# Kernel tuning notes

Measured on AMD Instinct MI355X. Metric: run time of the kernel, lower is better.

Reference implementation:

```python
import jax, jax.numpy as jnp
import numpy as np

# batch, nodes, input_dim, hid_dim, max_diffusion_step
B, N, C, D, K = 256, 512, 2, 64, 2


def setup_inputs() -> dict:
    key = jax.random.key(0)
    ks = jax.random.split(key, 7)
    F = C + D  # 66
    return {
        "inputs": jax.random.normal(ks[0], (B, N * C), jnp.float32),
        "state": jax.random.normal(ks[1], (B, N * D), jnp.float32),
        "adj": jax.random.uniform(ks[2], (N, N), jnp.float32),
        "W_gate": jax.random.normal(ks[3], (F * (K + 1), 2 * D), jnp.float32) * 0.05,
        "b_gate": jax.random.normal(ks[4], (2 * D,), jnp.float32) * 0.05,
        "W_cand": jax.random.normal(ks[5], (F * (K + 1), D), jnp.float32) * 0.05,
        "b_cand": jax.random.normal(ks[6], (D,), jnp.float32) * 0.05,
    }


def _diffusion_conv(x, adj, W, b):
    # x: (B, N, F) node features; Chebyshev-style diffusion basis then dense projection.
    b_, n_, f_ = x.shape
    k1 = W.shape[0] // f_  # num_matrices = max_diffusion_step + 1
    x0 = x.transpose(1, 2, 0).reshape(n_, f_ * b_)  # (N, F*B)
    xs = [x0]
    if k1 > 1:
        x1 = adj @ x0
        xs.append(x1)
        prev2, prev = x0, x1
        for _ in range(2, k1):
            cur = 2.0 * (adj @ prev) - prev2  # x2 = 2*adj@x1 - x0 recurrence
            xs.append(cur)
            prev2, prev = prev, cur
    stk = jnp.stack(xs, 0).reshape(k1, n_, f_, b_)  # (K+1, N, F, B)
    stk = stk.transpose(3, 1, 2, 0).reshape(b_ * n_, f_ * k1)  # (B*N, F*(K+1))
    out = stk @ W + b  # (B*N, O)
    return out.reshape(b_, n_ * W.shape[1])


def _random_walk_T(adj):
    a = adj + jnp.eye(adj.shape[0], dtype=adj.dtype)
    d = a.sum(axis=1)
    d_inv = jnp.where(d > 0, 1.0 / d, 0.0)
    return (d_inv[:, None] * a).T  # transposed random-walk matrix


def reference(inputs, state, adj, W_gate, b_gate, W_cand, b_cand):
    adj_rw = _random_walk_T(adj)
    inp3 = inputs.reshape(B, N, C)
    st3 = state.reshape(B, N, D)
    xg = jnp.concatenate([inp3, st3], axis=2)  # (B, N, C+D)
    value = jax.nn.sigmoid(_diffusion_conv(xg, adj_rw, W_gate, b_gate))
    value = value.reshape(B, N, 2 * D)
    r, u = value[..., :D], value[..., D:]
    u = u.reshape(B, N * D)
    xc = jnp.concatenate([inp3, r * st3], axis=2)
    c = jnp.tanh(_diffusion_conv(xc, adj_rw, W_cand, b_cand))  # (B, N*D)
    new_state = u * state + (1.0 - u) * c
    return new_state
```

## Files before the change

### kernel.cpp

```cpp
#include <hip/hip_runtime.h>
#include <math.h>

typedef unsigned short u16;
typedef float f32x4 __attribute__((ext_vector_type(4)));
typedef short s16x4 __attribute__((ext_vector_type(4)));
typedef short s16x8 __attribute__((ext_vector_type(8)));

#define AS3 __attribute__((address_space(3)))
#define AS1 __attribute__((address_space(1)))

__device__ __forceinline__ u16 f2bf(float f) {
  unsigned x = __builtin_bit_cast(unsigned, f);
  x += 0x7fffu + ((x >> 16) & 1u);
  return (u16)(x >> 16);
}
__device__ __forceinline__ float bf2f(u16 u) {
  unsigned x = ((unsigned)u) << 16;
  return __builtin_bit_cast(float, x);
}
__device__ __forceinline__ void gload16(const void* g, void* l) {
  __builtin_amdgcn_global_load_lds((const AS1 void*)g, (AS3 void*)l, 16, 0, 0);
}

__global__ void k_dinv(const float* __restrict__ adj, float* __restrict__ dinv) {
  int j = blockIdx.x;
  float s = 0.0f;
  for (int i = threadIdx.x; i < 512; i += 64) s += adj[(size_t)j * 512 + i];
  #pragma unroll
  for (int off = 32; off > 0; off >>= 1) s += __shfl_down(s, off);
  if (threadIdx.x == 0) dinv[j] = 1.0f / (1.0f + s);
}

__global__ void k_buildA(const float* __restrict__ adj, const float* __restrict__ dinv,
                         u16* __restrict__ Ab) {
  int i = blockIdx.x;
  for (int j = threadIdx.x; j < 512; j += 256) {
    float v = adj[(size_t)j * 512 + i] + ((i == j) ? 1.0f : 0.0f);
    Ab[(size_t)i * 512 + j] = f2bf(v * dinv[j]);
  }
}

__global__ __launch_bounds__(256) void k_prepST(const float* __restrict__ s,
                                                u16* __restrict__ Xn,
                                                u16* __restrict__ Xt) {
  __shared__ float Tl[64][65];
  const int b = blockIdx.y, n0 = blockIdx.x * 64;
  const int tid = threadIdx.x;
  const int r = tid >> 4, c4 = (tid & 15) * 4;
  #pragma unroll
  for (int i = 0; i < 4; ++i) {
    f32x4 v = *(const f32x4*)&s[((size_t)b * 512 + n0 + i * 16 + r) * 64 + c4];
    s16x4 o;
    #pragma unroll
    for (int j = 0; j < 4; ++j) { Tl[c4 + j][i * 16 + r] = v[j]; o[j] = (short)f2bf(v[j]); }
    *(s16x4*)&Xn[((size_t)b * 512 + n0 + i * 16 + r) * 64 + c4] = o;
  }
  __syncthreads();
  #pragma unroll
  for (int i = 0; i < 4; ++i) {
    int d = i * 16 + r;
    s16x4 o;
    #pragma unroll
    for (int j = 0; j < 4; ++j) o[j] = (short)f2bf(Tl[d][c4 + j]);
    *(s16x4*)&Xt[((size_t)b * 64 + d) * 512 + n0 + c4] = o;
  }
}

__global__ void k_prepI(const float* __restrict__ inp, u16* __restrict__ Xi0t) {
  const int b = blockIdx.x, t = threadIdx.x;
  const int m2 = t * 2;
  f32x4 v = *(const f32x4*)&inp[(size_t)b * 1024 + m2 * 2];
  unsigned p0 = (unsigned)f2bf(v.x) | ((unsigned)f2bf(v.z) << 16);
  unsigned p1 = (unsigned)f2bf(v.y) | ((unsigned)f2bf(v.w) << 16);
  *(unsigned*)&Xi0t[((size_t)b * 2 + 0) * 512 + m2] = p0;
  *(unsigned*)&Xi0t[((size_t)b * 2 + 1) * 512 + m2] = p1;
}

template<int NC>
__global__ void k_wtp(const float* __restrict__ W, u16* __restrict__ WTp) {
  int col = blockIdx.x, tid = threadIdx.x;
  if (tid >= 224) return;
  int kt = tid >> 5, g = (tid >> 3) & 3, j = tid & 7;
  int kappa = 32 * kt + 4 * g + ((j < 4) ? j : j + 12);
  float v = 0.0f;
  if (kappa < 192) {
    int f = kappa & 63, k1 = kappa >> 6;
    v = W[(size_t)((f + 2) * 3 + k1) * NC + col];
  } else if (kappa < 198) {
    int t = kappa - 192, k1 = t >> 1, c = t & 1;
    v = W[(size_t)(c * 3 + k1) * NC + col];
  }
  WTp[(size_t)col * 224 + tid] = f2bf(v);
}

template<int EPI, int WTB, int WNB>
__global__ __launch_bounds__(256, 3) void k_diffB(const u16* __restrict__ Xt,
                                                  const u16* __restrict__ Ab,
                                                  const u16* __restrict__ X0t,
                                                  u16* __restrict__ Yt,
                                                  u16* __restrict__ Yn) {
  __shared__ __align__(16) u16 SB[16384];
  const int tid = threadIdx.x;
  const int w = tid >> 6, l = tid & 63, g = l >> 4, l16 = l & 15;
  const int Rg = w >> 1, ng = w & 1;
  const int nt0 = blockIdx.x * 128;
  const size_t R0 = (size_t)blockIdx.y * 128;
  const bool isInput = (R0 >= 16384);
  f32x4 acc[4][4] = {};

#define STAGE(BUF, M0)                                                            \
  {                                                                               \
    _Pragma("unroll")                                                             \
    for (int i_ = 0; i_ < 2; ++i_) {                                              \
      int s_ = i_ * 256 + tid, r_ = s_ >> 2, p_ = s_ & 3;                         \
      gload16(&Xt[(R0 + r_) * 512 + (M0) + 8 * (p_ ^ (r_ & 3))],                  \
              &SB[(BUF) * 4096 + s_ * 8]);                                        \
      gload16(&Ab[(size_t)(nt0 + r_) * 512 + (M0) + 8 * (p_ ^ (r_ & 3))],         \
              &SB[8192 + (BUF) * 4096 + s_ * 8]);                                 \
    }                                                                             \
  }

  STAGE(0, 0);
  #pragma unroll
  for (int it = 0; it < 16; ++it) {
    const int cur = it & 1;
    if (it < 15) {
      if (cur == 0) STAGE(1, (it + 1) * 32)
      else          STAGE(0, (it + 1) * 32)
      asm volatile("s_waitcnt vmcnt(4)" ::: "memory");
    } else {
      asm volatile("s_waitcnt vmcnt(0)" ::: "memory");
    }
    __builtin_amdgcn_s_barrier();
    __builtin_amdgcn_sched_barrier(0);

    const u16* XL = &SB[cur * 4096];
    const u16* AL = &SB[8192 + cur * 4096];
    s16x8 af[4], bf[4];
    #pragma unroll
    for (int mt = 0; mt < 4; ++mt) {
      int r = Rg * 64 + mt * 16 + l16;
      const char* rowp = (const char*)XL + r * 64 + 8 * (g & 1);
      int c0 = (g >> 1), c1 = c0 + 2;
      s16x4 lo = *(const s16x4*)(rowp + 16 * (c0 ^ (r & 3)));
      s16x4 hi = *(const s16x4*)(rowp + 16 * (c1 ^ (r & 3)));
      af[mt] = __builtin_shufflevector(lo, hi, 0, 1, 2, 3, 4, 5, 6, 7);
    }
    #pragma unroll
    for (int nt = 0; nt < 4; ++nt) {
      int r = ng * 64 + nt * 16 + l16;
      const char* rowp = (const char*)AL + r * 64 + 8 * (g & 1);
      int c0 = (g >> 1), c1 = c0 + 2;
      s16x4 lo = *(const s16x4*)(rowp + 16 * (c0 ^ (r & 3)));
      s16x4 hi = *(const s16x4*)(rowp + 16 * (c1 ^ (r & 3)));
      bf[nt] = __builtin_shufflevector(lo, hi, 0, 1, 2, 3, 4, 5, 6, 7);
    }
    #pragma unroll
    for (int mt = 0; mt < 4; ++mt)
      #pragma unroll
      for (int nt = 0; nt < 4; ++nt)
        acc[mt][nt] = __builtin_amdgcn_mfma_f32_16x16x32_bf16(af[mt], bf[nt],
                                                              acc[mt][nt], 0, 0, 0);
    __builtin_amdgcn_s_barrier();
    __builtin_amdgcn_sched_barrier(0);
  }
#undef STAGE

  if (EPI) {
    #pragma unroll
    for (int i = 0; i < 8; ++i) {
      int s = i * 256 + tid, r = s >> 4, c = s & 15;
      gload16(&X0t[(R0 + r) * 512 + nt0 + c * 8], &SB[s * 8]);
    }
    asm volatile("s_waitcnt vmcnt(0)" ::: "memory");
    __builtin_amdgcn_s_barrier();
    #pragma unroll
    for (int mt = 0; mt < 4; ++mt)
      #pragma unroll
      for (int nt = 0; nt < 4; ++nt) {
        int nl = ng * 64 + nt * 16 + l16;
        #pragma unroll
        for (int rr = 0; rr < 4; ++rr) {
          int Rl = Rg * 64 + mt * 16 + 4 * g + rr;
          acc[mt][nt][rr] = 2.0f * acc[mt][nt][rr] - bf2f(SB[Rl * 128 + nl]);
        }
      }
  }

  if (WNB && !isInput) {
    #pragma unroll
    for (int mt = 0; mt < 4; ++mt)
      #pragma unroll
      for (int nt = 0; nt < 4; ++nt) {
        size_t R = R0 + Rg * 64 + mt * 16 + 4 * g;
        int n = nt0 + ng * 64 + nt * 16 + l16;
        s16x4 o;
        #pragma unroll
        for (int rr = 0; rr < 4; ++rr) o[rr] = (short)f2bf(acc[mt][nt][rr]);
        *(s16x4*)&Yn[((R >> 6) * 512 + n) * 64 + (R & 63)] = o;
      }
  }

  if (WTB || isInput) {
    if (EPI) __syncthreads();
    #pragma unroll
    for (int mt = 0; mt < 4; ++mt)
      #pragma unroll
      for (int nt = 0; nt < 4; ++nt) {
        int nl = ng * 64 + nt * 16 + l16;
        #pragma unroll
        for (int rr = 0; rr < 4; ++rr) {
          int Rl = Rg * 64 + mt * 16 + 4 * g + rr;
          SB[Rl * 128 + nl] = f2bf(acc[mt][nt][rr]);
        }
      }
    __syncthreads();
    #pragma unroll
    for (int i = 0; i < 8; ++i) {
      int s = i * 256 + tid, r = s >> 4, c = s & 15;
      *(s16x8*)&Yt[(R0 + r) * 512 + nt0 + c * 8] = *(const s16x8*)&SB[r * 128 + c * 8];
    }
  }
}

__global__ __launch_bounds__(256) void k_applyG(
    const u16* __restrict__ S0b, const u16* __restrict__ S1b, const u16* __restrict__ S2b,
    const float* __restrict__ inp, const u16* __restrict__ Yi1, const u16* __restrict__ Yi2,
    const u16* __restrict__ WTp, const float* __restrict__ bias,
    u16* __restrict__ XC0n, u16* __restrict__ XC0t, u16* __restrict__ Ub) {
  __shared__ __align__(16) u16 Sl[3][4096];
  __shared__ __align__(16) u16 St[64 * 36];
  const int tid = threadIdx.x;
  const int w = tid >> 6, l = tid & 63, g = l >> 4, l16 = l & 15;
  const int b = blockIdx.y, n0 = blockIdx.x * 64;
  const int colr = w * 16 + l16;

  const u16* Sb[3] = {S0b, S1b, S2b};
  #pragma unroll
  for (int k1 = 0; k1 < 3; ++k1)
    #pragma unroll
    for (int it = 0; it < 2; ++it) {
      int s = it * 256 + tid;
      int r = s >> 3, p = s & 7;
      gload16(&Sb[k1][((size_t)b * 512 + n0 + r) * 64 + 8 * (p ^ (r & 7))],
              &Sl[k1][(it * 256 + w * 64) * 8]);
    }
  s16x8 aw[7][2];
  {
    const u16* w0 = WTp + (size_t)colr * 224 + g * 8;
    const u16* w1 = WTp + (size_t)(colr + 64) * 224 + g * 8;
    #pragma unroll
    for (int kt = 0; kt < 7; ++kt) {
      aw[kt][0] = *(const s16x8*)&w0[kt * 32];
      aw[kt][1] = *(const s16x8*)&w1[kt * 32];
    }
  }
  for (int i = tid; i < 64 * 36; i += 256)
    if ((i % 36) >= 6) St[i] = 0;
  for (int t = tid; t < 384; t += 256) {
    int k1 = t >> 7, rr = (t >> 1) & 63, c = t & 1;
    u16 v;
    if (k1 == 0) v = f2bf(inp[((size_t)b * 512 + n0 + rr) * 2 + c]);
    else {
      const u16* Yk = (k1 == 1) ? Yi1 : Yi2;
      v = Yk[((size_t)b * 2 + c) * 512 + (n0 + rr)];
    }
    St[rr * 36 + k1 * 2 + c] = v;
  }
  asm volatile("s_waitcnt vmcnt(0)" ::: "memory");
  __syncthreads();

  f32x4 acc0[4] = {}, acc1[4] = {};
  #pragma unroll
  for (int kt = 0; kt < 7; ++kt) {
    #pragma unroll
    for (int ns = 0; ns < 4; ++ns) {
      int rn = ns * 16 + l16;
      s16x4 lo, hi;
      if (kt < 6) {
        const int buf = kt >> 1, ft = kt & 1;
        int c0 = ft * 4 + (g >> 1), c1 = c0 + 2;
        const char* rowp = (const char*)Sl[buf] + rn * 128 + 8 * (g & 1);
        lo = *(const s16x4*)(rowp + 16 * (c0 ^ (rn & 7)));
        hi = *(const s16x4*)(rowp + 16 * (c1 ^ (rn & 7)));
      } else {
        const char* rowp = (const char*)St + rn * 72 + 8 * g;
        lo = *(const s16x4*)(rowp);
        hi = *(const s16x4*)(rowp + 32);
      }
      s16x8 bs = __builtin_shufflevector(lo, hi, 0, 1, 2, 3, 4, 5, 6, 7);
      acc0[ns] = __builtin_amdgcn_mfma_f32_16x16x32_bf16(aw[kt][0], bs, acc0[ns], 0, 0, 0);
      acc1[ns] = __builtin_amdgcn_mfma_f32_16x16x32_bf16(aw[kt][1], bs, acc1[ns], 0, 0, 0);
    }
  }
  __syncthreads();

  f32x4 b4r = *(const f32x4*)&bias[w * 16 + 4 * g];
  f32x4 b4u = *(const f32x4*)&bias[64 + w * 16 + 4 * g];
  const int chk = 2 * w + (g >> 1);
  #pragma unroll
  for (int ns = 0; ns < 4; ++ns) {
    int rn = ns * 16 + l16;
    int n = n0 + rn;
    size_t base = ((size_t)b * 512 + n) * 64 + w * 16 + 4 * g;
    const char* srow = (const char*)Sl[0] + rn * 128 + 8 * (g & 1);
    s16x4 st4 = *(const s16x4*)(srow + 16 * (chk ^ (rn & 7)));
    s16x4 o;
    #pragma unroll
    for (int r = 0; r < 4; ++r) {
      float x = acc0[ns][r] + b4r[r];
      float sg = 1.0f / (1.0f + expf(-x));
      o[r] = (short)f2bf(sg * bf2f((u16)st4[r]));
    }
    *(s16x4*)&XC0n[base] = o;
    #pragma unroll
    for (int r = 0; r < 4; ++r)
      Sl[1][(w * 16 + 4 * g + r) * 64 + rn] = (u16)o[r];
    s16x4 uo;
    #pragma unroll
    for (int r = 0; r < 4; ++r) {
      float x = acc1[ns][r] + b4u[r];
      uo[r] = (short)f2bf(1.0f / (1.0f + expf(-x)));
    }
    *(s16x4*)&Ub[base] = uo;
  }
  __syncthreads();
  #pragma unroll
  for (int i = 0; i < 2; ++i) {
    int s = i * 256 + tid, f = s >> 3, c = s & 7;
    *(s16x8*)&XC0t[(size_t)(b * 64 + f) * 512 + n0 + c * 8] =
        *(const s16x8*)&Sl[1][f * 64 + c * 8];
  }
}

__global__ __launch_bounds__(256) void k_applyC(
    const u16* __restrict__ S0b, const u16* __restrict__ S1b, const u16* __restrict__ S2b,
    const float* __restrict__ inp, const u16* __restrict__ Yi1, const u16* __restrict__ Yi2,
    const u16* __restrict__ WTp, const float* __restrict__ bias,
    const float* __restrict__ state, const u16* __restrict__ Ub, float* __restrict__ outp) {
  __shared__ __align__(16) u16 Sl[3][4096];
  __shared__ __align__(16) u16 St[64 * 36];
  const int tid = threadIdx.x;
  const int w = tid >> 6, l = tid & 63, g = l >> 4, l16 = l & 15;
  const int b = blockIdx.y, n0 = blockIdx.x * 64;
  const int colr = w * 16 + l16;

  const u16* Sb[3] = {S0b, S1b, S2b};
  #pragma unroll
  for (int k1 = 0; k1 < 3; ++k1)
    #pragma unroll
    for (int it = 0; it < 2; ++it) {
      int s = it * 256 + tid;
      int r = s >> 3, p = s & 7;
      gload16(&Sb[k1][((size_t)b * 512 + n0 + r) * 64 + 8 * (p ^ (r & 7))],
              &Sl[k1][(it * 256 + w * 64) * 8]);
    }
  s16x8 aw[7];
  {
    const u16* w0 = WTp + (size_t)colr * 224 + g * 8;
    #pragma unroll
    for (int kt = 0; kt < 7; ++kt) aw[kt] = *(const s16x8*)&w0[kt * 32];
  }
  for (int i = tid; i < 64 * 36; i += 256)
    if ((i % 36) >= 6) St[i] = 0;
  for (int t = tid; t < 384; t += 256) {
    int k1 = t >> 7, rr = (t >> 1) & 63, c = t & 1;
    u16 v;
    if (k1 == 0) v = f2bf(inp[((size_t)b * 512 + n0 + rr) * 2 + c]);
    else {
      const u16* Yk = (k1 == 1) ? Yi1 : Yi2;
      v = Yk[((size_t)b * 2 + c) * 512 + (n0 + rr)];
    }
    St[rr * 36 + k1 * 2 + c] = v;
  }
  asm volatile("s_waitcnt vmcnt(0)" ::: "memory");
  __syncthreads();

  f32x4 acc[4] = {};
  #pragma unroll
  for (int kt = 0; kt < 7; ++kt) {
    #pragma unroll
    for (int ns = 0; ns < 4; ++ns) {
      int rn = ns * 16 + l16;
      s16x4 lo, hi;
      if (kt < 6) {
        const int buf = kt >> 1, ft = kt & 1;
        int c0 = ft * 4 + (g >> 1), c1 = c0 + 2;
        const char* rowp = (const char*)Sl[buf] + rn * 128 + 8 * (g & 1);
        lo = *(const s16x4*)(rowp + 16 * (c0 ^ (rn & 7)));
        hi = *(const s16x4*)(rowp + 16 * (c1 ^ (rn & 7)));
      } else {
        const char* rowp = (const char*)St + rn * 72 + 8 * g;
        lo = *(const s16x4*)(rowp);
        hi = *(const s16x4*)(rowp + 32);
      }
      s16x8 bs = __builtin_shufflevector(lo, hi, 0, 1, 2, 3, 4, 5, 6, 7);
      acc[ns] = __builtin_amdgcn_mfma_f32_16x16x32_bf16(aw[kt], bs, acc[ns], 0, 0, 0);
    }
  }

  f32x4 b4 = *(const f32x4*)&bias[w * 16 + 4 * g];
  #pragma unroll
  for (int ns = 0; ns < 4; ++ns) {
    int n = n0 + ns * 16 + l16;
    size_t base = ((size_t)b * 512 + n) * 64 + w * 16 + 4 * g;
    s16x4 ub4 = *(const s16x4*)&Ub[base];
    f32x4 st4 = *(const f32x4*)&state[base];
    f32x4 o;
    #pragma unroll
    for (int r = 0; r < 4; ++r) {
      float c = tanhf(acc[ns][r] + b4[r]);
      float u = bf2f((u16)ub4[r]);
      o[r] = fmaf(u, st4[r] - c, c);
    }
    *(f32x4*)&outp[base] = o;
  }
}

extern "C" void kernel_launch(void* const* d_in, const int* in_sizes, int n_in,
                              void* d_out, int out_size, void* d_ws, size_t ws_size,
                              hipStream_t stream) {
  const float* inp   = (const float*)d_in[0];
  const float* state = (const float*)d_in[1];
  const float* adj   = (const float*)d_in[2];
  const float* Wg    = (const float*)d_in[3];
  const float* bg    = (const float*)d_in[4];
  const float* Wc    = (const float*)d_in[5];
  const float* bc    = (const float*)d_in[6];
  float* out = (float*)d_out;

  char* p = (char*)d_ws;
  u16* Abf    = (u16*)p; p += 524288;
  u16* XAll0t = (u16*)p; p += 17301504;
  u16* X1t    = (u16*)p; p += 17301504;
  u16* Yi2t   = (u16*)p; p += 524288;
  u16* WTpg   = (u16*)p; p += 57344;
  u16* WTpc   = (u16*)p; p += 28672;
  float* dinv = (float*)p; p += 2048;
  u16* XG0n   = (u16*)p; p += 16777216;
  u16* XC0n   = (u16*)p; p += 16777216;
  u16* X1n    = (u16*)p; p += 16777216;
  u16* X2n    = (u16*)p; p += 16777216;
  u16* Xi0t   = XAll0t + (size_t)16384 * 512;
  u16* XC0t   = XAll0t;
  u16* Yi1t   = X1t + (size_t)16384 * 512;
  u16* Yi2off = Yi2t - (size_t)16384 * 512;
  u16* Ub     = XG0n;

  k_dinv   <<<512, 64,  0, stream>>>(adj, dinv);
  k_buildA <<<512, 256, 0, stream>>>(adj, dinv, Abf);
  k_prepST <<<dim3(8, 256), 256, 0, stream>>>(state, XG0n, XAll0t);
  k_prepI  <<<256, 256, 0, stream>>>(inp, Xi0t);
  k_wtp<128><<<128, 256, 0, stream>>>(Wg, WTpg);
  k_wtp<64> <<<64, 256, 0, stream>>>(Wc, WTpc);

  k_diffB<0, 1, 1><<<dim3(4, 132), 256, 0, stream>>>(XAll0t, Abf, nullptr, X1t, X1n);
  k_diffB<1, 0, 1><<<dim3(4, 132), 256, 0, stream>>>(X1t, Abf, XAll0t, Yi2off, X2n);
  k_applyG<<<dim3(8, 256), 256, 0, stream>>>(XG0n, X1n, X2n, inp, Yi1t, Yi2t,
                                             WTpg, bg, XC0n, XC0t, Ub);

  k_diffB<0, 1, 1><<<dim3(4, 128), 256, 0, stream>>>(XC0t, Abf, nullptr, X1t, X1n);
  k_diffB<1, 0, 1><<<dim3(4, 128), 256, 0, stream>>>(X1t, Abf, XC0t, Yi2off, X2n);
  k_applyC<<<dim3(8, 256), 256, 0, stream>>>(XC0n, X1n, X2n, inp, Yi1t, Yi2t,
                                             WTpc, bc, state, Ub, out);
}
```

Before: 202.9 us.

## Fold Chebyshev recurrence into weights and fuse second diffusion with projection

```diff
diff --git a/kernel.cpp b/kernel.cpp
--- a/kernel.cpp
+++ b/kernel.cpp
@@ -85,18 +85,23 @@
   float v = 0.0f;
   if (kappa < 192) {
     int f = kappa & 63, k1 = kappa >> 6;
-    v = W[(size_t)((f + 2) * 3 + k1) * NC + col];
+    const float* base = &W[(size_t)((f + 2) * 3) * NC + col];
+    v = (k1 == 0) ? base[0] - base[2 * NC]
+      : (k1 == 1) ? base[1 * NC]
+                  : 2.0f * base[2 * NC];
   } else if (kappa < 198) {
     int t = kappa - 192, k1 = t >> 1, c = t & 1;
-    v = W[(size_t)(c * 3 + k1) * NC + col];
+    const float* base = &W[(size_t)(c * 3) * NC + col];
+    v = (k1 == 0) ? base[0] - base[2 * NC]
+      : (k1 == 1) ? base[1 * NC]
+                  : 2.0f * base[2 * NC];
   }
   WTp[(size_t)col * 224 + tid] = f2bf(v);
 }
 
-template<int EPI, int WTB, int WNB>
+template<int WTB, int WNB>
 __global__ __launch_bounds__(256, 3) void k_diffB(const u16* __restrict__ Xt,
                                                   const u16* __restrict__ Ab,
-                                                  const u16* __restrict__ X0t,
                                                   u16* __restrict__ Yt,
                                                   u16* __restrict__ Yn) {
   __shared__ __align__(16) u16 SB[16384];
@@ -166,27 +171,6 @@
   }
 #undef STAGE
 
-  if (EPI) {
-    #pragma unroll
-    for (int i = 0; i < 8; ++i) {
-      int s = i * 256 + tid, r = s >> 4, c = s & 15;
-      gload16(&X0t[(R0 + r) * 512 + nt0 + c * 8], &SB[s * 8]);
-    }
-    asm volatile("s_waitcnt vmcnt(0)" ::: "memory");
-    __builtin_amdgcn_s_barrier();
-    #pragma unroll
-    for (int mt = 0; mt < 4; ++mt)
-      #pragma unroll
-      for (int nt = 0; nt < 4; ++nt) {
-        int nl = ng * 64 + nt * 16 + l16;
-        #pragma unroll
-        for (int rr = 0; rr < 4; ++rr) {
-          int Rl = Rg * 64 + mt * 16 + 4 * g + rr;
-          acc[mt][nt][rr] = 2.0f * acc[mt][nt][rr] - bf2f(SB[Rl * 128 + nl]);
-        }
-      }
-  }
-
   if (WNB && !isInput) {
     #pragma unroll
     for (int mt = 0; mt < 4; ++mt)
@@ -202,7 +186,6 @@
   }
 
   if (WTB || isInput) {
-    if (EPI) __syncthreads();
     #pragma unroll
     for (int mt = 0; mt < 4; ++mt)
       #pragma unroll
@@ -223,197 +206,244 @@
   }
 }
 
-__global__ __launch_bounds__(256) void k_applyG(
-    const u16* __restrict__ S0b, const u16* __restrict__ S1b, const u16* __restrict__ S2b,
+template<int ISGATE>
+__global__ __launch_bounds__(256, 2) void k_fuse(
+    const u16* __restrict__ Xt, const u16* __restrict__ Ab,
+    const u16* __restrict__ S0src, const u16* __restrict__ S1src,
     const float* __restrict__ inp, const u16* __restrict__ Yi1, const u16* __restrict__ Yi2,
     const u16* __restrict__ WTp, const float* __restrict__ bias,
-    u16* __restrict__ XC0n, u16* __restrict__ XC0t, u16* __restrict__ Ub) {
-  __shared__ __align__(16) u16 Sl[3][4096];
-  __shared__ __align__(16) u16 St[64 * 36];
+    const u16* __restrict__ SnState, const float* __restrict__ statef,
+    const u16* __restrict__ Ubin,
+    u16* __restrict__ XC0n, u16* __restrict__ XC0t, u16* __restrict__ Ubout,
+    float* __restrict__ outp) {
+  __shared__ __align__(16) u16 SB[32768];
   const int tid = threadIdx.x;
   const int w = tid >> 6, l = tid & 63, g = l >> 4, l16 = l & 15;
-  const int b = blockIdx.y, n0 = blockIdx.x * 64;
-  const int colr = w * 16 + l16;
-
-  const u16* Sb[3] = {S0b, S1b, S2b};
-  #pragma unroll
-  for (int k1 = 0; k1 < 3; ++k1)
-    #pragma unroll
-    for (int it = 0; it < 2; ++it) {
-      int s = it * 256 + tid;
-      int r = s >> 3, p = s & 7;
-      gload16(&Sb[k1][((size_t)b * 512 + n0 + r) * 64 + 8 * (p ^ (r & 7))],
-              &Sl[k1][(it * 256 + w * 64) * 8]);
-    }
-  s16x8 aw[7][2];
-  {
-    const u16* w0 = WTp + (size_t)colr * 224 + g * 8;
-    const u16* w1 = WTp + (size_t)(colr + 64) * 224 + g * 8;
+  const int Rg = w >> 1, ng = w & 1;
+  const int nt0 = blockIdx.x * 128;
+  const size_t R0 = (size_t)blockIdx.y * 128;
+  f32x4 facc[4][4] = {};
+
+#define FSTAGE(BUF, M0)                                                           \
+  {                                                                               \
+    _Pragma("unroll")                                                             \
+    for (int i_ = 0; i_ < 2; ++i_) {                                              \
+      int s_ = i_ * 256 + tid, r_ = s_ >> 2, p_ = s_ & 3;                         \
+      gload16(&Xt[(R0 + r_) * 512 + (M0) + 8 * (p_ ^ (r_ & 3))],                  \
+              &SB[(BUF) * 4096 + s_ * 8]);                                        \
+      gload16(&Ab[(size_t)(nt0 + r_) * 512 + (M0) + 8 * (p_ ^ (r_ & 3))],         \
+              &SB[8192 + (BUF) * 4096 + s_ * 8]);                                 \
+    }                                                                             \
+  }
+
+  FSTAGE(0, 0);
+  #pragma unroll
+  for (int it = 0; it < 16; ++it) {
+    const int cur = it & 1;
+    if (it < 15) {
+      if (cur == 0) FSTAGE(1, (it + 1) * 32)
+      else          FSTAGE(0, (it + 1) * 32)
+      asm volatile("s_waitcnt vmcnt(4)" ::: "memory");
+    } else {
+      asm volatile("s_waitcnt vmcnt(0)" ::: "memory");
+    }
+    __builtin_amdgcn_s_barrier();
+    __builtin_amdgcn_sched_barrier(0);
+
+    const u16* XL = &SB[cur * 4096];
+    const u16* AL = &SB[8192 + cur * 4096];
+    s16x8 af[4], bf[4];
+    #pragma unroll
+    for (int mt = 0; mt < 4; ++mt) {
+      int r = Rg * 64 + mt * 16 + l16;
+      const char* rowp = (const char*)XL + r * 64 + 8 * (g & 1);
+      int c0 = (g >> 1), c1 = c0 + 2;
+      s16x4 lo = *(const s16x4*)(rowp + 16 * (c0 ^ (r & 3)));
+      s16x4 hi = *(const s16x4*)(rowp + 16 * (c1 ^ (r & 3)));
+      af[mt] = __builtin_shufflevector(lo, hi, 0, 1, 2, 3, 4, 5, 6, 7);
+    }
+    #pragma unroll
+    for (int nt = 0; nt < 4; ++nt) {
+      int r = ng * 64 + nt * 16 + l16;
+      const char* rowp = (const char*)AL + r * 64 + 8 * (g & 1);
+      int c0 = (g >> 1), c1 = c0 + 2;
+      s16x4 lo = *(const s16x4*)(rowp + 16 * (c0 ^ (r & 3)));
+      s16x4 hi = *(const s16x4*)(rowp + 16 * (c1 ^ (r & 3)));
+      bf[nt] = __builtin_shufflevector(lo, hi, 0, 1, 2, 3, 4, 5, 6, 7);
+    }
+    #pragma unroll
+    for (int mt = 0; mt < 4; ++mt)
+      #pragma unroll
+      for (int nt = 0; nt < 4; ++nt)
+        facc[mt][nt] = __builtin_amdgcn_mfma_f32_16x16x32_bf16(af[mt], bf[nt],
+                                                               facc[mt][nt], 0, 0, 0);
+    __builtin_amdgcn_s_barrier();
+    __builtin_amdgcn_sched_barrier(0);
+  }
+#undef FSTAGE
+
+  constexpr int NCF = ISGATE ? 2 : 1;
+  s16x8 aw[7][NCF];
+  #pragma unroll
+  for (int cf = 0; cf < NCF; ++cf) {
+    const u16* wp = WTp + (size_t)((ISGATE ? w * 32 : w * 16) + cf * 16 + l16) * 224 + g * 8;
+    #pragma unroll
+    for (int kt = 0; kt < 7; ++kt) aw[kt][cf] = *(const s16x8*)&wp[kt * 32];
+  }
+
+  #pragma unroll
+  for (int bb = 0; bb < 2; ++bb) {
+    const int b = (int)(R0 >> 6) + bb;
+    if (bb == 0) {
+      #pragma unroll
+      for (int it = 0; it < 4; ++it) {
+        int s = it * 256 + tid, r = s >> 3, p = s & 7;
+        size_t gidx = ((size_t)b * 512 + nt0 + r) * 64 + 8 * (p ^ (r & 7));
+        gload16(&S0src[gidx], &SB[16384 + (it * 256 + w * 64) * 8]);
+        gload16(&S1src[gidx], &SB[0 + (it * 256 + w * 64) * 8]);
+      }
+      for (int i = tid; i < 4608; i += 256)
+        if ((i % 36) >= 6) SB[8192 + i] = 0;
+    }
+    for (int t = tid; t < 768; t += 256) {
+      int p = t >> 7, nn = t & 127;
+      int k1 = p >> 1, c = p & 1;
+      int n = nt0 + nn;
+      u16 v;
+      if (k1 == 0) v = f2bf(inp[(size_t)b * 1024 + n * 2 + c]);
+      else v = ((k1 == 1) ? Yi1 : Yi2)[((size_t)b * 2 + c) * 512 + n];
+      SB[8192 + nn * 36 + p] = v;
+    }
+    if (Rg == bb) {
+      #pragma unroll
+      for (int mt = 0; mt < 4; ++mt)
+        #pragma unroll
+        for (int nt = 0; nt < 4; ++nt) {
+          int nl = ng * 64 + nt * 16 + l16;
+          #pragma unroll
+          for (int rr = 0; rr < 4; ++rr) {
+            int f = mt * 16 + 4 * g + rr;
+            int cc = f >> 3;
+            SB[24576 + nl * 64 + ((cc ^ (nl & 7)) << 3) + (f & 7)] =
+                f2bf(facc[mt][nt][rr]);
+          }
+        }
+    }
+    asm volatile("s_waitcnt vmcnt(0)" ::: "memory");
+    __syncthreads();
+
+    f32x4 aacc[NCF][8];
+    #pragma unroll
+    for (int cf = 0; cf < NCF; ++cf)
+      #pragma unroll
+      for (int ns = 0; ns < 8; ++ns) aacc[cf][ns] = f32x4{0.f, 0.f, 0.f, 0.f};
     #pragma unroll
     for (int kt = 0; kt < 7; ++kt) {
-      aw[kt][0] = *(const s16x8*)&w0[kt * 32];
-      aw[kt][1] = *(const s16x8*)&w1[kt * 32];
-    }
-  }
-  for (int i = tid; i < 64 * 36; i += 256)
-    if ((i % 36) >= 6) St[i] = 0;
-  for (int t = tid; t < 384; t += 256) {
-    int k1 = t >> 7, rr = (t >> 1) & 63, c = t & 1;
-    u16 v;
-    if (k1 == 0) v = f2bf(inp[((size_t)b * 512 + n0 + rr) * 2 + c]);
-    else {
-      const u16* Yk = (k1 == 1) ? Yi1 : Yi2;
-      v = Yk[((size_t)b * 2 + c) * 512 + (n0 + rr)];
-    }
-    St[rr * 36 + k1 * 2 + c] = v;
-  }
-  asm volatile("s_waitcnt vmcnt(0)" ::: "memory");
-  __syncthreads();
-
-  f32x4 acc0[4] = {}, acc1[4] = {};
-  #pragma unroll
-  for (int kt = 0; kt < 7; ++kt) {
-    #pragma unroll
-    for (int ns = 0; ns < 4; ++ns) {
-      int rn = ns * 16 + l16;
-      s16x4 lo, hi;
-      if (kt < 6) {
-        const int buf = kt >> 1, ft = kt & 1;
-        int c0 = ft * 4 + (g >> 1), c1 = c0 + 2;
-        const char* rowp = (const char*)Sl[buf] + rn * 128 + 8 * (g & 1);
-        lo = *(const s16x4*)(rowp + 16 * (c0 ^ (rn & 7)));
-        hi = *(const s16x4*)(rowp + 16 * (c1 ^ (rn & 7)));
+      #pragma unroll
+      for (int ns = 0; ns < 8; ++ns) {
+        int rn = ns * 16 + l16;
+        s16x4 lo, hi;
+        if (kt < 6) {
+          int off = (kt < 2) ? 16384 : (kt < 4) ? 0 : 24576;
+          int ft = kt & 1;
+          const char* rowp = (const char*)&SB[off] + rn * 128 + 8 * (g & 1);
+          int c0 = ft * 4 + (g >> 1), c1 = c0 + 2;
+          lo = *(const s16x4*)(rowp + 16 * (c0 ^ (rn & 7)));
+          hi = *(const s16x4*)(rowp + 16 * (c1 ^ (rn & 7)));
+        } else {
+          const char* rowp = (const char*)&SB[8192] + rn * 72 + 8 * g;
+          lo = *(const s16x4*)rowp;
+          hi = *(const s16x4*)(rowp + 32);
+        }
+        s16x8 bs = __builtin_shufflevector(lo, hi, 0, 1, 2, 3, 4, 5, 6, 7);
+        #pragma unroll
+        for (int cf = 0; cf < NCF; ++cf)
+          aacc[cf][ns] = __builtin_amdgcn_mfma_f32_16x16x32_bf16(aw[kt][cf], bs,
+                                                                 aacc[cf][ns], 0, 0, 0);
+      }
+    }
+    __syncthreads();
+
+    if (bb == 0) {
+      #pragma unroll
+      for (int it = 0; it < 4; ++it) {
+        int s = it * 256 + tid, r = s >> 3, p = s & 7;
+        size_t gidx = ((size_t)(b + 1) * 512 + nt0 + r) * 64 + 8 * (p ^ (r & 7));
+        gload16(&S0src[gidx], &SB[16384 + (it * 256 + w * 64) * 8]);
+        gload16(&S1src[gidx], &SB[0 + (it * 256 + w * 64) * 8]);
+      }
+    }
+
+    if (ISGATE) {
+      if (w < 2) {
+        #pragma unroll
+        for (int cf = 0; cf < NCF; ++cf) {
+          int col0 = w * 32 + cf * 16 + 4 * g;
+          f32x4 b4 = *(const f32x4*)&bias[col0];
+          #pragma unroll
+          for (int ns = 0; ns < 8; ++ns) {
+            int nl = ns * 16 + l16;
+            size_t base = ((size_t)b * 512 + nt0 + nl) * 64 + col0;
+            s16x4 st4 = *(const s16x4*)&SnState[base];
+            s16x4 o;
+            #pragma unroll
+            for (int rr = 0; rr < 4; ++rr) {
+              float x = aacc[cf][ns][rr] + b4[rr];
+              float sg = 1.0f / (1.0f + expf(-x));
+              o[rr] = (short)f2bf(sg * bf2f((u16)st4[rr]));
+            }
+            *(s16x4*)&XC0n[base] = o;
+            #pragma unroll
+            for (int rr = 0; rr < 4; ++rr)
+              SB[24576 + (col0 + rr) * 128 + nl] = (u16)o[rr];
+          }
+        }
       } else {
-        const char* rowp = (const char*)St + rn * 72 + 8 * g;
-        lo = *(const s16x4*)(rowp);
-        hi = *(const s16x4*)(rowp + 32);
-      }
-      s16x8 bs = __builtin_shufflevector(lo, hi, 0, 1, 2, 3, 4, 5, 6, 7);
-      acc0[ns] = __builtin_amdgcn_mfma_f32_16x16x32_bf16(aw[kt][0], bs, acc0[ns], 0, 0, 0);
-      acc1[ns] = __builtin_amdgcn_mfma_f32_16x16x32_bf16(aw[kt][1], bs, acc1[ns], 0, 0, 0);
-    }
-  }
-  __syncthreads();
-
-  f32x4 b4r = *(const f32x4*)&bias[w * 16 + 4 * g];
-  f32x4 b4u = *(const f32x4*)&bias[64 + w * 16 + 4 * g];
-  const int chk = 2 * w + (g >> 1);
-  #pragma unroll
-  for (int ns = 0; ns < 4; ++ns) {
-    int rn = ns * 16 + l16;
-    int n = n0 + rn;
-    size_t base = ((size_t)b * 512 + n) * 64 + w * 16 + 4 * g;
-    const char* srow = (const char*)Sl[0] + rn * 128 + 8 * (g & 1);
-    s16x4 st4 = *(const s16x4*)(srow + 16 * (chk ^ (rn & 7)));
-    s16x4 o;
-    #pragma unroll
-    for (int r = 0; r < 4; ++r) {
-      float x = acc0[ns][r] + b4r[r];
-      float sg = 1.0f / (1.0f + expf(-x));
-      o[r] = (short)f2bf(sg * bf2f((u16)st4[r]));
-    }
-    *(s16x4*)&XC0n[base] = o;
-    #pragma unroll
-    for (int r = 0; r < 4; ++r)
-      Sl[1][(w * 16 + 4 * g + r) * 64 + rn] = (u16)o[r];
-    s16x4 uo;
-    #pragma unroll
-    for (int r = 0; r < 4; ++r) {
-      float x = acc1[ns][r] + b4u[r];
-      uo[r] = (short)f2bf(1.0f / (1.0f + expf(-x)));
-    }
-    *(s16x4*)&Ub[base] = uo;
-  }
-  __syncthreads();
-  #pragma unroll
-  for (int i = 0; i < 2; ++i) {
-    int s = i * 256 + tid, f = s >> 3, c = s & 7;
-    *(s16x8*)&XC0t[(size_t)(b * 64 + f) * 512 + n0 + c * 8] =
-        *(const s16x8*)&Sl[1][f * 64 + c * 8];
-  }
-}
-
-__global__ __launch_bounds__(256) void k_applyC(
-    const u16* __restrict__ S0b, const u16* __restrict__ S1b, const u16* __restrict__ S2b,
-    const float* __restrict__ inp, const u16* __restrict__ Yi1, const u16* __restrict__ Yi2,
-    const u16* __restrict__ WTp, const float* __restrict__ bias,
-    const float* __restrict__ state, const u16* __restrict__ Ub, float* __restrict__ outp) {
-  __shared__ __align__(16) u16 Sl[3][4096];
-  __shared__ __align__(16) u16 St[64 * 36];
-  const int tid = threadIdx.x;
-  const int w = tid >> 6, l = tid & 63, g = l >> 4, l16 = l & 15;
-  const int b = blockIdx.y, n0 = blockIdx.x * 64;
-  const int colr = w * 16 + l16;
-
-  const u16* Sb[3] = {S0b, S1b, S2b};
-  #pragma unroll
-  for (int k1 = 0; k1 < 3; ++k1)
-    #pragma unroll
-    for (int it = 0; it < 2; ++it) {
-      int s = it * 256 + tid;
-      int r = s >> 3, p = s & 7;
-      gload16(&Sb[k1][((size_t)b * 512 + n0 + r) * 64 + 8 * (p ^ (r & 7))],
-              &Sl[k1][(it * 256 + w * 64) * 8]);
-    }
-  s16x8 aw[7];
-  {
-    const u16* w0 = WTp + (size_t)colr * 224 + g * 8;
-    #pragma unroll
-    for (int kt = 0; kt < 7; ++kt) aw[kt] = *(const s16x8*)&w0[kt * 32];
-  }
-  for (int i = tid; i < 64 * 36; i += 256)
-    if ((i % 36) >= 6) St[i] = 0;
-  for (int t = tid; t < 384; t += 256) {
-    int k1 = t >> 7, rr = (t >> 1) & 63, c = t & 1;
-    u16 v;
-    if (k1 == 0) v = f2bf(inp[((size_t)b * 512 + n0 + rr) * 2 + c]);
-    else {
-      const u16* Yk = (k1 == 1) ? Yi1 : Yi2;
-      v = Yk[((size_t)b * 2 + c) * 512 + (n0 + rr)];
-    }
-    St[rr * 36 + k1 * 2 + c] = v;
-  }
-  asm volatile("s_waitcnt vmcnt(0)" ::: "memory");
-  __syncthreads();
-
-  f32x4 acc[4] = {};
-  #pragma unroll
-  for (int kt = 0; kt < 7; ++kt) {
-    #pragma unroll
-    for (int ns = 0; ns < 4; ++ns) {
-      int rn = ns * 16 + l16;
-      s16x4 lo, hi;
-      if (kt < 6) {
-        const int buf = kt >> 1, ft = kt & 1;
-        int c0 = ft * 4 + (g >> 1), c1 = c0 + 2;
-        const char* rowp = (const char*)Sl[buf] + rn * 128 + 8 * (g & 1);
-        lo = *(const s16x4*)(rowp + 16 * (c0 ^ (rn & 7)));
-        hi = *(const s16x4*)(rowp + 16 * (c1 ^ (rn & 7)));
-      } else {
-        const char* rowp = (const char*)St + rn * 72 + 8 * g;
-        lo = *(const s16x4*)(rowp);
-        hi = *(const s16x4*)(rowp + 32);
-      }
-      s16x8 bs = __builtin_shufflevector(lo, hi, 0, 1, 2, 3, 4, 5, 6, 7);
-      acc[ns] = __builtin_amdgcn_mfma_f32_16x16x32_bf16(aw[kt], bs, acc[ns], 0, 0, 0);
-    }
-  }
-
-  f32x4 b4 = *(const f32x4*)&bias[w * 16 + 4 * g];
-  #pragma unroll
-  for (int ns = 0; ns < 4; ++ns) {
-    int n = n0 + ns * 16 + l16;
-    size_t base = ((size_t)b * 512 + n) * 64 + w * 16 + 4 * g;
-    s16x4 ub4 = *(const s16x4*)&Ub[base];
-    f32x4 st4 = *(const f32x4*)&state[base];
-    f32x4 o;
-    #pragma unroll
-    for (int r = 0; r < 4; ++r) {
-      float c = tanhf(acc[ns][r] + b4[r]);
-      float u = bf2f((u16)ub4[r]);
-      o[r] = fmaf(u, st4[r] - c, c);
-    }
-    *(f32x4*)&outp[base] = o;
+        #pragma unroll
+        for (int cf = 0; cf < NCF; ++cf) {
+          int col0 = w * 32 + cf * 16 + 4 * g;
+          f32x4 b4 = *(const f32x4*)&bias[col0];
+          #pragma unroll
+          for (int ns = 0; ns < 8; ++ns) {
+            int n = nt0 + ns * 16 + l16;
+            size_t base = ((size_t)b * 512 + n) * 64 + (col0 - 64);
+            s16x4 uo;
+            #pragma unroll
+            for (int rr = 0; rr < 4; ++rr) {
+              float x = aacc[cf][ns][rr] + b4[rr];
+              uo[rr] = (short)f2bf(1.0f / (1.0f + expf(-x)));
+            }
+            *(s16x4*)&Ubout[base] = uo;
+          }
+        }
+      }
+      __syncthreads();
+      #pragma unroll
+      for (int i2 = 0; i2 < 4; ++i2) {
+        int s = i2 * 256 + tid, f = s >> 4, cc = s & 15;
+        *(s16x8*)&XC0t[((size_t)b * 64 + f) * 512 + nt0 + cc * 8] =
+            *(const s16x8*)&SB[24576 + f * 128 + cc * 8];
+      }
+      __syncthreads();
+    } else {
+      int col0 = w * 16 + 4 * g;
+      f32x4 b4 = *(const f32x4*)&bias[col0];
+      #pragma unroll
+      for (int ns = 0; ns < 8; ++ns) {
+        int n = nt0 + ns * 16 + l16;
+        size_t base = ((size_t)b * 512 + n) * 64 + col0;
+        s16x4 ub4 = *(const s16x4*)&Ubin[base];
+        f32x4 st4 = *(const f32x4*)&statef[base];
+        f32x4 o;
+        #pragma unroll
+        for (int rr = 0; rr < 4; ++rr) {
+          float c = tanhf(aacc[0][ns][rr] + b4[rr]);
+          float u = bf2f((u16)ub4[rr]);
+          o[rr] = fmaf(u, st4[rr] - c, c);
+        }
+        *(f32x4*)&outp[base] = o;
+      }
+    }
   }
 }
 
@@ -440,12 +470,10 @@
   u16* XG0n   = (u16*)p; p += 16777216;
   u16* XC0n   = (u16*)p; p += 16777216;
   u16* X1n    = (u16*)p; p += 16777216;
-  u16* X2n    = (u16*)p; p += 16777216;
+  u16* Ub     = (u16*)p; p += 16777216;
   u16* Xi0t   = XAll0t + (size_t)16384 * 512;
   u16* XC0t   = XAll0t;
   u16* Yi1t   = X1t + (size_t)16384 * 512;
-  u16* Yi2off = Yi2t - (size_t)16384 * 512;
-  u16* Ub     = XG0n;
 
   k_dinv   <<<512, 64,  0, stream>>>(adj, dinv);
   k_buildA <<<512, 256, 0, stream>>>(adj, dinv, Abf);
@@ -454,13 +482,13 @@
   k_wtp<128><<<128, 256, 0, stream>>>(Wg, WTpg);
   k_wtp<64> <<<64, 256, 0, stream>>>(Wc, WTpc);
 
-  k_diffB<0, 1, 1><<<dim3(4, 132), 256, 0, stream>>>(XAll0t, Abf, nullptr, X1t, X1n);
-  k_diffB<1, 0, 1><<<dim3(4, 132), 256, 0, stream>>>(X1t, Abf, XAll0t, Yi2off, X2n);
-  k_applyG<<<dim3(8, 256), 256, 0, stream>>>(XG0n, X1n, X2n, inp, Yi1t, Yi2t,
-                                             WTpg, bg, XC0n, XC0t, Ub);
-
-  k_diffB<0, 1, 1><<<dim3(4, 128), 256, 0, stream>>>(XC0t, Abf, nullptr, X1t, X1n);
-  k_diffB<1, 0, 1><<<dim3(4, 128), 256, 0, stream>>>(X1t, Abf, XC0t, Yi2off, X2n);
-  k_applyC<<<dim3(8, 256), 256, 0, stream>>>(XC0n, X1n, X2n, inp, Yi1t, Yi2t,
-                                             WTpc, bc, state, Ub, out);
-}
+  k_diffB<1, 1><<<dim3(4, 132), 256, 0, stream>>>(XAll0t, Abf, X1t, X1n);
+  k_diffB<1, 0><<<dim3(4, 4), 256, 0, stream>>>(Yi1t, Abf, Yi2t, nullptr);
+  k_fuse<1><<<dim3(4, 128), 256, 0, stream>>>(X1t, Abf, XG0n, X1n, inp, Yi1t, Yi2t,
+                                              WTpg, bg, XG0n, nullptr, nullptr,
+                                              XC0n, XC0t, Ub, nullptr);
+  k_diffB<1, 1><<<dim3(4, 128), 256, 0, stream>>>(XC0t, Abf, X1t, X1n);
+  k_fuse<0><<<dim3(4, 128), 256, 0, stream>>>(X1t, Abf, XC0n, X1n, inp, Yi1t, Yi2t,
+                                              WTpc, bc, nullptr, state, Ub,
+                                              nullptr, nullptr, nullptr, out);
+}
```

Result: slower. 332.9 us (+64.1%).
